# Kernel tuning notes

Hardware: AMD Instinct MI355X
Metric: run time of the kernel (lower is better)

Reference implementation:

```python
import jax, jax.numpy as jnp
import numpy as np

K = 4  # recurrent_kernel_size


def setup_inputs() -> dict:
    key = jax.random.key(0)
    k1, k2, k3, k4 = jax.random.split(key, 4)
    b, t, d = 4, 4096, 1024
    x = jax.random.normal(k1, (b, t, d), dtype=jnp.float32)
    W_conv = jax.random.normal(k2, (d, 1, K), dtype=jnp.float32) * (1.0 / np.sqrt(K))
    W_proj = jax.random.normal(k3, (4 * d, d), dtype=jnp.float32) * (1.0 / np.sqrt(d))
    W_out = jax.random.normal(k4, (d, d), dtype=jnp.float32) * (1.0 / np.sqrt(d))
    return {"x": x, "W_conv": W_conv, "W_proj": W_proj, "W_out": W_out}


def _causal_dwconv(x_btd, W_conv):
    # x: [b,t,d]; W_conv: [d,1,k] (torch depthwise layout). Causal: left-pad k-1.
    d = x_btd.shape[-1]
    x_bdt = jnp.transpose(x_btd, (0, 2, 1))  # [b,d,t]
    y = jax.lax.conv_general_dilated(
        x_bdt, W_conv,
        window_strides=(1,),
        padding=[(K - 1, 0)],
        feature_group_count=d,
        dimension_numbers=("NCH", "OIH", "NCH"),
    )
    return jnp.transpose(y, (0, 2, 1))  # [b,t,d]


def reference(x, W_conv, W_proj, W_out):
    b, t, d = x.shape
    mixed = _causal_dwconv(x, W_conv)
    u = jnp.einsum("btd,ed->bte", x + mixed, W_proj)  # [b,t,4d]
    v, gate, decay, inject = jnp.split(u, 4, axis=-1)
    gate = jax.nn.sigmoid(gate)
    decay = jax.nn.sigmoid(decay)
    inject = jnp.tanh(inject)

    def step(state, inp):
        dec_t, inj_t, g_t, v_t = inp  # each [b,d]
        state = dec_t * state + (1.0 - dec_t) * inj_t
        out = g_t * v_t + (1.0 - g_t) * state
        return state, out

    # move time to leading axis for scan: [t,b,d]
    seq = (jnp.swapaxes(decay, 0, 1), jnp.swapaxes(inject, 0, 1),
           jnp.swapaxes(gate, 0, 1), jnp.swapaxes(v, 0, 1))
    state0 = jnp.zeros((b, d), dtype=x.dtype)
    _, y_tbd = jax.lax.scan(step, state0, seq)
    y = jnp.swapaxes(y_tbd, 0, 1)  # [b,t,d]
    return jnp.einsum("btd,ed->bte", y, W_out)
```

## Files before the change

### kernel.cpp

```cpp
#include <hip/hip_runtime.h>
#include <hip/hip_bf16.h>
#include <math.h>

typedef __hip_bfloat16 bf16;
typedef __bf16 bf16x8 __attribute__((ext_vector_type(8)));
typedef float f32x4 __attribute__((ext_vector_type(4)));
typedef float f32x4v __attribute__((ext_vector_type(4)));
typedef unsigned short u16x8v __attribute__((ext_vector_type(8)));
typedef unsigned short u16x4v __attribute__((ext_vector_type(4)));

#define BB 4
#define TT 4096
#define DD 1024

__device__ __forceinline__ float fast_sigmoid(float x) {
  return 1.0f / (1.0f + __expf(-x));
}
__device__ __forceinline__ float fast_tanh(float x) {
  return 2.0f / (1.0f + __expf(-2.0f * x)) - 1.0f;
}
__device__ __forceinline__ float b2f(unsigned short u) {
  union { unsigned int i; float f; } x;
  x.i = ((unsigned int)u) << 16;
  return x.f;
}
__device__ __forceinline__ unsigned short f2b(float f) {
  union { bf16 h; unsigned short u; } x;
  x.h = __float2bfloat16(f);
  return x.u;
}

__global__ __launch_bounds__(256) void w2bf_kernel(const float* __restrict__ w,
                                                   bf16* __restrict__ o,
                                                   int n) {
  int i = blockIdx.x * 256 + threadIdx.x;
  if (i < n) o[i] = __float2bfloat16(w[i]);
}

__global__ __launch_bounds__(256) void conv_add_kernel(
    const float* __restrict__ x, const float* __restrict__ Wc,
    bf16* __restrict__ xm, int total4) {
  int i = blockIdx.x * 256 + threadIdx.x;
  if (i >= total4) return;
  int c4 = (i & (DD / 4 - 1)) * 4;
  int t = (i / (DD / 4)) % TT;
  size_t base = (size_t)i * 4;
  f32x4v x0 = *(const f32x4v*)(x + base);
  f32x4v p1 = (t >= 1) ? *(const f32x4v*)(x + base - DD) : (f32x4v)0.0f;
  f32x4v p2 = (t >= 2) ? *(const f32x4v*)(x + base - 2 * DD) : (f32x4v)0.0f;
  f32x4v p3 = (t >= 3) ? *(const f32x4v*)(x + base - 3 * DD) : (f32x4v)0.0f;
  u16x4v o;
#pragma unroll
  for (int j = 0; j < 4; ++j) {
    f32x4v w = *(const f32x4v*)(Wc + (size_t)(c4 + j) * 4);
    float acc = x0[j] + w[3] * x0[j] + w[2] * p1[j] + w[1] * p2[j] +
                w[0] * p3[j];
    o[j] = f2b(acc);
  }
  *(u16x4v*)(xm + base) = o;
}

template <int EP>
__global__ __launch_bounds__(512) void gemm256_kernel(
    const bf16* __restrict__ A, const bf16* __restrict__ B,
    void* __restrict__ C, int M, int N, int K, int MB) {
  __shared__ __align__(16) bf16 As[2][2][128][64];
  __shared__ __align__(16) bf16 Bs[2][2][128][64];

  const int tid = threadIdx.x;
  const int wv = tid >> 6, l = tid & 63;
  const int wm = wv >> 2, wn = wv & 3;

  const int bid = blockIdx.x;
  const int xcd = bid & 7, ii = bid >> 3;
  const int mb8 = MB >> 3;
  const int bm = xcd * mb8 + (ii % mb8);
  const int bn = ii / mb8;
  const int m0 = bm * 256, n0 = bn * 256;

  const int lr3 = l >> 3;
  const int gcolE = ((l & 7) ^ (l >> 3)) * 8;
  const int l15 = l & 15;
  const int rxor = (l15 & 7) << 3;
  const int lhi8 = (l >> 4) * 8;
  const int colK[2] = {lhi8 ^ rxor, (32 + lhi8) ^ rxor};

  const bf16* Arow = A + (size_t)(m0 + wv * 16 + lr3) * K + gcolE;
  const bf16* Brow = B + (size_t)(n0 + wv * 16 + lr3) * K + gcolE;

  auto stage = [&](int ht) {
    const int kt = ht >> 2, which = ht & 3;
    const int slot = kt & 1;
    const int k0 = kt * 64;
    if (which < 2) {
      const int half = which;
#pragma unroll
      for (int j = 0; j < 2; ++j) {
        const bf16* src = Brow + (size_t)(half * 128 + j * 8) * K + k0;
        __builtin_amdgcn_global_load_lds(
            (const __attribute__((address_space(1))) void*)src,
            (__attribute__((address_space(3))) void*)(&Bs[slot][half][0][0] +
                                                      wv * 1024 + j * 512),
            16, 0, 0);
      }
    } else {
      const int half = which - 2;
#pragma unroll
      for (int j = 0; j < 2; ++j) {
        const bf16* src = Arow + (size_t)(half * 128 + j * 8) * K + k0;
        __builtin_amdgcn_global_load_lds(
            (const __attribute__((address_space(1))) void*)src,
            (__attribute__((address_space(3))) void*)(&As[slot][half][0][0] +
                                                      wv * 1024 + j * 512),
            16, 0, 0);
      }
    }
  };

  f32x4 acc[8][4];
#pragma unroll
  for (int i = 0; i < 8; ++i)
#pragma unroll
    for (int j = 0; j < 4; ++j) acc[i][j] = (f32x4)0.0f;

  const int NT2 = K >> 7;
  const int nht = (K >> 6) * 4;

#pragma unroll
  for (int h = 0; h < 6; ++h) stage(h);
  asm volatile("s_waitcnt vmcnt(4)" ::: "memory");
  __builtin_amdgcn_s_barrier();

  bf16x8 aF[4][2], bF0[2][2], bF1[2][2];

#pragma unroll 1
  for (int t = 0; t < NT2; ++t) {
#pragma unroll
    for (int g = 0; g < 8; ++g) {
      const int q = g & 3, grp = g >> 2;
      const bf16* ar = &As[grp][wm][0][0];
      const bf16* br = &Bs[grp][wn >> 1][0][0] + (wn & 1) * 4096;
      if (q == 0) {
#pragma unroll
        for (int mi = 0; mi < 4; ++mi)
#pragma unroll
          for (int ks = 0; ks < 2; ++ks)
            aF[mi][ks] =
                *(const bf16x8*)(ar + (mi * 16 + l15) * 64 + colK[ks]);
#pragma unroll
        for (int ni = 0; ni < 2; ++ni)
#pragma unroll
          for (int ks = 0; ks < 2; ++ks)
            bF0[ni][ks] =
                *(const bf16x8*)(br + (ni * 16 + l15) * 64 + colK[ks]);
      } else if (q == 1) {
#pragma unroll
        for (int ni = 0; ni < 2; ++ni)
#pragma unroll
          for (int ks = 0; ks < 2; ++ks)
            bF1[ni][ks] =
                *(const bf16x8*)(br + ((ni + 2) * 16 + l15) * 64 + colK[ks]);
      } else if (q == 2) {
#pragma unroll
        for (int mi = 0; mi < 4; ++mi)
#pragma unroll
          for (int ks = 0; ks < 2; ++ks)
            aF[mi][ks] =
                *(const bf16x8*)(ar + ((mi + 4) * 16 + l15) * 64 + colK[ks]);
      }
      {
        const int ht = 8 * t + 6 + g;
        if (ht < nht) stage(ht);
      }
      __builtin_amdgcn_sched_barrier(0);
      __builtin_amdgcn_s_barrier();
      __builtin_amdgcn_s_setprio(1);
#pragma unroll
      for (int mi = 0; mi < 4; ++mi)
#pragma unroll
        for (int nj = 0; nj < 2; ++nj)
#pragma unroll
          for (int ks = 0; ks < 2; ++ks)
            acc[mi + (q >= 2 ? 4 : 0)][nj + ((q & 1) ? 2 : 0)] =
                __builtin_amdgcn_mfma_f32_16x16x32_bf16(
                    aF[mi][ks], (q & 1) ? bF1[nj][ks] : bF0[nj][ks],
                    acc[mi + (q >= 2 ? 4 : 0)][nj + ((q & 1) ? 2 : 0)], 0, 0,
                    0);
      __builtin_amdgcn_s_setprio(0);
      if (g == 3) {
        if (t == NT2 - 1)
          asm volatile("s_waitcnt vmcnt(0)" ::: "memory");
        else
          asm volatile("s_waitcnt vmcnt(4)" ::: "memory");
      } else if (g == 7) {
        asm volatile("s_waitcnt vmcnt(4)" ::: "memory");
      }
      __builtin_amdgcn_sched_barrier(0);
      __builtin_amdgcn_s_barrier();
    }
  }

#pragma unroll
  for (int mi = 0; mi < 8; ++mi) {
    const int row = m0 + wm * 128 + mi * 16 + (l >> 4) * 4;
#pragma unroll
    for (int ni = 0; ni < 4; ++ni) {
      const int col = n0 + wn * 64 + ni * 16 + l15;
#pragma unroll
      for (int j = 0; j < 4; ++j) {
        float v = acc[mi][ni][j];
        if (EP == 0) {
          ((float*)C)[(size_t)(row + j) * N + col] = v;
        } else {
          const int cls = col >> 10;
          if (cls == 1 || cls == 2) v = fast_sigmoid(v);
          else if (cls == 3) v = fast_tanh(v);
          ((bf16*)C)[(size_t)(row + j) * N + col] = __float2bfloat16(v);
        }
      }
    }
  }
}

#define BM 64
#define BN 64
#define BKK 16
__global__ __launch_bounds__(256) void gemm_nt_kernel(
    const bf16* __restrict__ A, const float* __restrict__ B,
    float* __restrict__ C, int M, int N, int K) {
  __shared__ float Asm[BKK][BM + 1];
  __shared__ float Bsm[BKK][BN + 1];
  const int n0 = blockIdx.x * BN;
  const int m0 = blockIdx.y * BM;
  const int tid = threadIdx.x;
  const int tx = tid & 15, ty = tid >> 4;
  const int lk = tid & 15, lr = tid >> 4;
  float acc[4][4] = {};
  for (int k0 = 0; k0 < K; k0 += BKK) {
#pragma unroll
    for (int p = 0; p < 4; ++p) {
      Asm[lk][lr + 16 * p] =
          __bfloat162float(A[(size_t)(m0 + lr + 16 * p) * K + (k0 + lk)]);
      Bsm[lk][lr + 16 * p] = B[(size_t)(n0 + lr + 16 * p) * K + (k0 + lk)];
    }
    __syncthreads();
#pragma unroll
    for (int kk = 0; kk < BKK; ++kk) {
      float a[4], b[4];
#pragma unroll
      for (int i = 0; i < 4; ++i) a[i] = Asm[kk][ty * 4 + i];
#pragma unroll
      for (int j = 0; j < 4; ++j) b[j] = Bsm[kk][tx * 4 + j];
#pragma unroll
      for (int i = 0; i < 4; ++i)
#pragma unroll
        for (int j = 0; j < 4; ++j) acc[i][j] += a[i] * b[j];
    }
    __syncthreads();
  }
#pragma unroll
  for (int i = 0; i < 4; ++i)
#pragma unroll
    for (int j = 0; j < 4; ++j)
      C[(size_t)(m0 + ty * 4 + i) * N + (n0 + tx * 4 + j)] = acc[i][j];
}

__global__ __launch_bounds__(256) void scan_chunk_kernel(
    const bf16* __restrict__ u, float* __restrict__ cA,
    float* __restrict__ cB, int nchunk, int tchunk) {
  int idx = blockIdx.x * 256 + threadIdx.x;
  int c8 = (idx & (DD / 8 - 1)) * 8;
  int chunk = (idx / (DD / 8)) % nchunk;
  int b = idx / ((DD / 8) * nchunk);
  const bf16* ub = u + (size_t)b * TT * 4 * DD;
  float Aacc[8], Bacc[8];
#pragma unroll
  for (int j = 0; j < 8; ++j) { Aacc[j] = 1.0f; Bacc[j] = 0.0f; }
  int t0 = chunk * tchunk;
  for (int t = t0; t < t0 + tchunk; ++t) {
    const bf16* row = ub + (size_t)t * 4 * DD;
    u16x8v dv = *(const u16x8v*)(row + 2 * DD + c8);
    u16x8v iv = *(const u16x8v*)(row + 3 * DD + c8);
#pragma unroll
    for (int j = 0; j < 8; ++j) {
      float dec = b2f(dv[j]), inj = b2f(iv[j]);
      Aacc[j] *= dec;
      Bacc[j] = dec * Bacc[j] + (1.0f - dec) * inj;
    }
  }
  int base = (b * nchunk + chunk) * DD + c8;
#pragma unroll
  for (int j = 0; j < 8; ++j) { cA[base + j] = Aacc[j]; cB[base + j] = Bacc[j]; }
}

__global__ __launch_bounds__(256) void scan_prefix_kernel(
    const float* __restrict__ cA, const float* __restrict__ cB,
    float* __restrict__ S, int nchunk) {
  int idx = blockIdx.x * 256 + threadIdx.x;
  int c = idx % DD;
  int b = idx / DD;
  float s = 0.0f;
  for (int j = 0; j < nchunk; ++j) {
    int e = (b * nchunk + j) * DD + c;
    S[e] = s;
    s = cA[e] * s + cB[e];
  }
}

__global__ __launch_bounds__(256) void scan_out_kernel(
    const bf16* __restrict__ u, const float* __restrict__ S,
    bf16* __restrict__ y, int nchunk, int tchunk) {
  int idx = blockIdx.x * 256 + threadIdx.x;
  int c8 = (idx & (DD / 8 - 1)) * 8;
  int chunk = (idx / (DD / 8)) % nchunk;
  int b = idx / ((DD / 8) * nchunk);
  const bf16* ub = u + (size_t)b * TT * 4 * DD;
  bf16* yb = y + (size_t)b * TT * DD;
  float st[8];
  int sbase = (b * nchunk + chunk) * DD + c8;
#pragma unroll
  for (int j = 0; j < 8; ++j) st[j] = S[sbase + j];
  int t0 = chunk * tchunk;
  for (int t = t0; t < t0 + tchunk; ++t) {
    const bf16* row = ub + (size_t)t * 4 * DD;
    u16x8v vv = *(const u16x8v*)(row + c8);
    u16x8v gv = *(const u16x8v*)(row + DD + c8);
    u16x8v dv = *(const u16x8v*)(row + 2 * DD + c8);
    u16x8v iv = *(const u16x8v*)(row + 3 * DD + c8);
    u16x8v ov;
#pragma unroll
    for (int j = 0; j < 8; ++j) {
      float dec = b2f(dv[j]), inj = b2f(iv[j]);
      float g = b2f(gv[j]), v = b2f(vv[j]);
      st[j] = dec * st[j] + (1.0f - dec) * inj;
      ov[j] = f2b(g * v + (1.0f - g) * st[j]);
    }
    *(u16x8v*)(yb + (size_t)t * DD + c8) = ov;
  }
}

extern "C" void kernel_launch(void* const* d_in, const int* in_sizes, int n_in,
                              void* d_out, int out_size, void* d_ws,
                              size_t ws_size, hipStream_t stream) {
  const float* x = (const float*)d_in[0];
  const float* Wc = (const float*)d_in[1];
  const float* Wp = (const float*)d_in[2];
  const float* Wo = (const float*)d_in[3];
  float* out = (float*)d_out;

  const size_t nb = (size_t)TT * DD;

  auto need = [&](int nbat, int nchunk, bool wob) -> size_t {
    return (size_t)nbat * nb * 2 + (size_t)nbat * 4 * nb * 2 +
           (size_t)4 * DD * DD * 2 + (wob ? (size_t)DD * DD * 2 : 0) +
           (size_t)3 * nbat * nchunk * DD * 4;
  };

  int nbat, nchunk;
  bool haveWob;
  if (ws_size >= need(4, 64, true)) {
    nbat = 4; nchunk = 64; haveWob = true;
  } else if (ws_size >= need(1, 64, true)) {
    nbat = 1; nchunk = 64; haveWob = true;
  } else {
    nbat = 1; nchunk = 16; haveWob = false;
  }
  const int tchunk = TT / nchunk;

  char* p = (char*)d_ws;
  bf16* Wpb = (bf16*)p;  p += (size_t)4 * DD * DD * 2;
  bf16* Wob = nullptr;
  if (haveWob) { Wob = (bf16*)p; p += (size_t)DD * DD * 2; }
  bf16* xm = (bf16*)p;   p += (size_t)nbat * nb * 2;
  bf16* u = (bf16*)p;    p += (size_t)nbat * 4 * nb * 2;
  float* cA = (float*)p; p += (size_t)nbat * nchunk * DD * 4;
  float* cB = (float*)p; p += (size_t)nbat * nchunk * DD * 4;
  float* S = (float*)p;
  bf16* y = xm;

  w2bf_kernel<<<(4 * DD * DD) / 256, 256, 0, stream>>>(Wp, Wpb, 4 * DD * DD);
  if (haveWob)
    w2bf_kernel<<<(DD * DD) / 256, 256, 0, stream>>>(Wo, Wob, DD * DD);

  for (int b0 = 0; b0 < BB; b0 += nbat) {
    const float* xb = x + (size_t)b0 * nb;
    float* outb = out + (size_t)b0 * nb;
    const int Mtot = nbat * TT;
    const int total4 = (int)(nbat * nb / 4);

    conv_add_kernel<<<total4 / 256, 256, 0, stream>>>(xb, Wc, xm, total4);

    {
      const int MB = Mtot / 256;
      const int nwg = MB * (4 * DD / 256);
      gemm256_kernel<1><<<nwg, 512, 0, stream>>>(xm, Wpb, u, Mtot, 4 * DD, DD,
                                                 MB);
    }
    {
      int nthreads = nbat * nchunk * (DD / 8);
      scan_chunk_kernel<<<nthreads / 256, 256, 0, stream>>>(u, cA, cB, nchunk,
                                                            tchunk);
      scan_prefix_kernel<<<(nbat * DD) / 256, 256, 0, stream>>>(cA, cB, S,
                                                                nchunk);
      scan_out_kernel<<<nthreads / 256, 256, 0, stream>>>(u, S, y, nchunk,
                                                          tchunk);
    }
    if (haveWob) {
      const int MB = Mtot / 256;
      const int nwg = MB * (DD / 256);
      gemm256_kernel<0><<<nwg, 512, 0, stream>>>(y, Wob, outb, Mtot, DD, DD,
                                                 MB);
    } else {
      dim3 grid(DD / BN, Mtot / BM);
      gemm_nt_kernel<<<grid, 256, 0, stream>>>(y, Wo, outb, Mtot, DD, DD);
    }
  }
}
```

Before: 318.0 us.

## Deepen GEMM prefetch pipeline and precompute LDS byte offsets

Restructures the 256x256 GEMM load schedule so seven quarter-tile stages are in flight instead of six, and waits at vmcnt(6). The stage lambda becomes a simpler per-quarter load with precomputed row pointers. LDS fragment addresses are now precomputed byte offsets, which cuts integer address math. The MFMA loop order is changed to iterate ks outermost, and the launch bounds now request 2 blocks per CU. The goal is to hide more global latency and trim VALU overhead, at the cost of register pressure from the occupancy hint and possible hazards from the reordered barriers and waitcnts.

```diff
diff --git a/kernel.cpp b/kernel.cpp
--- a/kernel.cpp
+++ b/kernel.cpp
@@ -61,7 +61,7 @@
 }
 
 template <int EP>
-__global__ __launch_bounds__(512) void gemm256_kernel(
+__global__ __launch_bounds__(512, 2) void gemm256_kernel(
     const bf16* __restrict__ A, const bf16* __restrict__ B,
     void* __restrict__ C, int M, int N, int K, int MB) {
   __shared__ __align__(16) bf16 As[2][2][128][64];
@@ -83,37 +83,37 @@
   const int l15 = l & 15;
   const int rxor = (l15 & 7) << 3;
   const int lhi8 = (l >> 4) * 8;
-  const int colK[2] = {lhi8 ^ rxor, (32 + lhi8) ^ rxor};
+  const int colK0 = lhi8 ^ rxor;
+  const int colK1 = (32 + lhi8) ^ rxor;
+
+  const char* AsB = (const char*)&As[0][0][0][0];
+  const char* BsB = (const char*)&Bs[0][0][0][0];
+  const int aB0 = wm * 16384 + l15 * 128 + colK0 * 2;
+  const int aB1 = wm * 16384 + l15 * 128 + colK1 * 2;
+  const int bB0 = (wn >> 1) * 16384 + (wn & 1) * 8192 + l15 * 128 + colK0 * 2;
+  const int bB1 = (wn >> 1) * 16384 + (wn & 1) * 8192 + l15 * 128 + colK1 * 2;
 
   const bf16* Arow = A + (size_t)(m0 + wv * 16 + lr3) * K + gcolE;
   const bf16* Brow = B + (size_t)(n0 + wv * 16 + lr3) * K + gcolE;
-
-  auto stage = [&](int ht) {
-    const int kt = ht >> 2, which = ht & 3;
-    const int slot = kt & 1;
-    const int k0 = kt * 64;
-    if (which < 2) {
-      const int half = which;
-#pragma unroll
-      for (int j = 0; j < 2; ++j) {
-        const bf16* src = Brow + (size_t)(half * 128 + j * 8) * K + k0;
-        __builtin_amdgcn_global_load_lds(
-            (const __attribute__((address_space(1))) void*)src,
-            (__attribute__((address_space(3))) void*)(&Bs[slot][half][0][0] +
-                                                      wv * 1024 + j * 512),
-            16, 0, 0);
-      }
-    } else {
-      const int half = which - 2;
-#pragma unroll
-      for (int j = 0; j < 2; ++j) {
-        const bf16* src = Arow + (size_t)(half * 128 + j * 8) * K + k0;
-        __builtin_amdgcn_global_load_lds(
-            (const __attribute__((address_space(1))) void*)src,
-            (__attribute__((address_space(3))) void*)(&As[slot][half][0][0] +
-                                                      wv * 1024 + j * 512),
-            16, 0, 0);
-      }
+  const bf16* ArowH = Arow + (size_t)128 * K;
+  const bf16* BrowH = Brow + (size_t)128 * K;
+
+  bf16* AsW = &As[0][0][0][0];
+  bf16* BsW = &Bs[0][0][0][0];
+
+  auto stage1 = [&](int which, int k0) {
+    const int slot = (k0 >> 6) & 1;
+    const bf16* src0 =
+        (which == 0 ? Brow : which == 1 ? BrowH : which == 2 ? Arow : ArowH) +
+        k0;
+    bf16* dst0 = (which < 2 ? BsW : AsW) + slot * 16384 + (which & 1) * 8192 +
+                 wv * 1024;
+#pragma unroll
+    for (int j = 0; j < 2; ++j) {
+      __builtin_amdgcn_global_load_lds(
+          (const __attribute__((address_space(1))) void*)(src0 +
+                                                          (size_t)(j * 8) * K),
+          (__attribute__((address_space(3))) void*)(dst0 + j * 512), 16, 0, 0);
     }
   };
 
@@ -124,78 +124,69 @@
     for (int j = 0; j < 4; ++j) acc[i][j] = (f32x4)0.0f;
 
   const int NT2 = K >> 7;
-  const int nht = (K >> 6) * 4;
-
-#pragma unroll
-  for (int h = 0; h < 6; ++h) stage(h);
-  asm volatile("s_waitcnt vmcnt(4)" ::: "memory");
+
+  stage1(0, 0); stage1(1, 0); stage1(2, 0); stage1(3, 0);
+  stage1(0, 64); stage1(1, 64); stage1(2, 64);
+  asm volatile("s_waitcnt vmcnt(6)" ::: "memory");
   __builtin_amdgcn_s_barrier();
 
   bf16x8 aF[4][2], bF0[2][2], bF1[2][2];
 
+  int kb = 0;
 #pragma unroll 1
-  for (int t = 0; t < NT2; ++t) {
+  for (int t = 0; t < NT2; ++t, kb += 128) {
 #pragma unroll
     for (int g = 0; g < 8; ++g) {
       const int q = g & 3, grp = g >> 2;
-      const bf16* ar = &As[grp][wm][0][0];
-      const bf16* br = &Bs[grp][wn >> 1][0][0] + (wn & 1) * 4096;
+      const int gof = grp * 32768;
       if (q == 0) {
 #pragma unroll
-        for (int mi = 0; mi < 4; ++mi)
-#pragma unroll
-          for (int ks = 0; ks < 2; ++ks)
-            aF[mi][ks] =
-                *(const bf16x8*)(ar + (mi * 16 + l15) * 64 + colK[ks]);
-#pragma unroll
-        for (int ni = 0; ni < 2; ++ni)
-#pragma unroll
-          for (int ks = 0; ks < 2; ++ks)
-            bF0[ni][ks] =
-                *(const bf16x8*)(br + (ni * 16 + l15) * 64 + colK[ks]);
+        for (int mi = 0; mi < 4; ++mi) {
+          aF[mi][0] = *(const bf16x8*)(AsB + aB0 + gof + mi * 2048);
+          aF[mi][1] = *(const bf16x8*)(AsB + aB1 + gof + mi * 2048);
+        }
+#pragma unroll
+        for (int ni = 0; ni < 2; ++ni) {
+          bF0[ni][0] = *(const bf16x8*)(BsB + bB0 + gof + ni * 2048);
+          bF0[ni][1] = *(const bf16x8*)(BsB + bB1 + gof + ni * 2048);
+        }
       } else if (q == 1) {
 #pragma unroll
-        for (int ni = 0; ni < 2; ++ni)
-#pragma unroll
-          for (int ks = 0; ks < 2; ++ks)
-            bF1[ni][ks] =
-                *(const bf16x8*)(br + ((ni + 2) * 16 + l15) * 64 + colK[ks]);
+        for (int ni = 0; ni < 2; ++ni) {
+          bF1[ni][0] = *(const bf16x8*)(BsB + bB0 + gof + (ni + 2) * 2048);
+          bF1[ni][1] = *(const bf16x8*)(BsB + bB1 + gof + (ni + 2) * 2048);
+        }
       } else if (q == 2) {
 #pragma unroll
-        for (int mi = 0; mi < 4; ++mi)
-#pragma unroll
-          for (int ks = 0; ks < 2; ++ks)
-            aF[mi][ks] =
-                *(const bf16x8*)(ar + ((mi + 4) * 16 + l15) * 64 + colK[ks]);
+        for (int mi = 0; mi < 4; ++mi) {
+          aF[mi][0] = *(const bf16x8*)(AsB + aB0 + gof + (mi + 4) * 2048);
+          aF[mi][1] = *(const bf16x8*)(AsB + aB1 + gof + (mi + 4) * 2048);
+        }
       }
-      {
-        const int ht = 8 * t + 6 + g;
-        if (ht < nht) stage(ht);
-      }
+      if (t < NT2 - 1 || g == 0)
+        stage1((7 + g) & 3, kb + 64 * ((7 + g) >> 2));
       __builtin_amdgcn_sched_barrier(0);
       __builtin_amdgcn_s_barrier();
       __builtin_amdgcn_s_setprio(1);
 #pragma unroll
-      for (int mi = 0; mi < 4; ++mi)
-#pragma unroll
-        for (int nj = 0; nj < 2; ++nj)
-#pragma unroll
-          for (int ks = 0; ks < 2; ++ks)
+      for (int ks = 0; ks < 2; ++ks)
+#pragma unroll
+        for (int mi = 0; mi < 4; ++mi)
+#pragma unroll
+          for (int nj = 0; nj < 2; ++nj)
             acc[mi + (q >= 2 ? 4 : 0)][nj + ((q & 1) ? 2 : 0)] =
                 __builtin_amdgcn_mfma_f32_16x16x32_bf16(
                     aF[mi][ks], (q & 1) ? bF1[nj][ks] : bF0[nj][ks],
                     acc[mi + (q >= 2 ? 4 : 0)][nj + ((q & 1) ? 2 : 0)], 0, 0,
                     0);
       __builtin_amdgcn_s_setprio(0);
-      if (g == 3) {
-        if (t == NT2 - 1)
+      if (q == 3) {
+        if (g == 3 && t == NT2 - 1)
           asm volatile("s_waitcnt vmcnt(0)" ::: "memory");
         else
-          asm volatile("s_waitcnt vmcnt(4)" ::: "memory");
-      } else if (g == 7) {
-        asm volatile("s_waitcnt vmcnt(4)" ::: "memory");
+          asm volatile("s_waitcnt vmcnt(6)" ::: "memory");
+        __builtin_amdgcn_sched_barrier(0);
       }
-      __builtin_amdgcn_sched_barrier(0);
       __builtin_amdgcn_s_barrier();
     }
   }
```

Result: no change. 315.7 us (-0.7%).
